# Kernel tuning notes

Hardware: AMD Instinct MI355X
Metric: run time of the kernel (lower is better)

Reference implementation:

```python
import jax, jax.numpy as jnp
import numpy as np

IN_DIM, HIDDEN, NCLASS = 128, 512, 10
BETA, THRESH = 0.9, 0.15


def setup_inputs() -> dict:
    key = jax.random.key(0)
    k_x, k_w1, k_w2 = jax.random.split(key, 3)
    B, T = 512, 512
    x = jax.random.uniform(k_x, (B, T, IN_DIM), dtype=jnp.float32)
    # kaiming_normal_(nonlinearity='linear'): std = 1/sqrt(fan_in); fc1 then scaled by 0.8
    W1 = jax.random.normal(k_w1, (HIDDEN, IN_DIM), dtype=jnp.float32) * (0.8 / np.sqrt(IN_DIM))
    b1 = jnp.zeros((HIDDEN,), dtype=jnp.float32)
    W2 = jax.random.normal(k_w2, (NCLASS, HIDDEN), dtype=jnp.float32) * (1.0 / np.sqrt(HIDDEN))
    b2 = jnp.zeros((NCLASS,), dtype=jnp.float32)
    return {"x": x, "W1": W1, "b1": b1, "W2": W2, "b2": b2}


def reference(x, W1, b1, W2, b2):
    B, T, D = x.shape
    xs = jnp.transpose(2.0 * x, (1, 0, 2))  # [T, B, D]

    def step(carry, xt):
        mem, acc = carry
        cur = xt @ W1.T + b1                      # [B, H]
        reset = (mem > THRESH).astype(cur.dtype)  # spike from previous mem (snntorch order)
        mem = BETA * mem + cur - reset * THRESH   # subtract reset
        spk = (mem > THRESH).astype(cur.dtype)
        acc = acc + spk @ W2.T + b2               # [B, C]
        return (mem, acc), None

    mem0 = jnp.zeros((B, HIDDEN), dtype=jnp.float32)
    acc0 = jnp.zeros((B, NCLASS), dtype=jnp.float32)
    (_, acc), _ = jax.lax.scan(step, (mem0, acc0), xs)
    return acc / T
```

## Files before the change

### kernel.cpp

```cpp
#include <hip/hip_runtime.h>

#define IN_DIM  128
#define HIDDEN  512
#define NCLASS  10
#define TSTEPS  512
#define BATCH   512
#define BETA    0.9f
#define THRESH  0.15f

typedef __attribute__((ext_vector_type(8))) short bf16x8;
typedef __attribute__((ext_vector_type(4))) float f32x4;

__device__ __forceinline__ unsigned short f2bf_rne(float f) {
    unsigned int u = __float_as_uint(f);
    u += 0x7FFFu + ((u >> 16) & 1u);
    return (unsigned short)(u >> 16);
}
__device__ __forceinline__ float bf2f(unsigned short h) {
    return __uint_as_float(((unsigned int)h) << 16);
}

__device__ __forceinline__ bf16x8 cvt8(const float4 a, const float4 b, float s) {
    float v[8] = {a.x * s, a.y * s, a.z * s, a.w * s,
                  b.x * s, b.y * s, b.z * s, b.w * s};
    bf16x8 o;
#pragma unroll
    for (int e = 0; e < 8; ++e) o[e] = (short)f2bf_rne(v[e]);
    return o;
}

__device__ __forceinline__ void cvt8s(const float4 a, const float4 b,
                                      bf16x8* hi, bf16x8* lo) {
    float v[8] = {a.x, a.y, a.z, a.w, b.x, b.y, b.z, b.w};
#pragma unroll
    for (int e = 0; e < 8; ++e) {
        unsigned short h = f2bf_rne(v[e]);
        (*hi)[e] = (short)h;
        (*lo)[e] = (short)f2bf_rne(v[e] - bf2f(h));
    }
}

__global__ __launch_bounds__(256, 4) void conv_x3(
    const float* __restrict__ x, unsigned short* __restrict__ xt)
{
    const int bid  = blockIdx.x;
    const int bblk = bid >> 9;
    const int t    = bid & 511;
    const int g    = threadIdx.x;
    const int kf   = g >> 6;
    const int i    = g & 63;
    const int l15  = i & 15;
    const int lg   = i >> 4;

    const float* src = x + ((size_t)(bblk * 16 + l15) * TSTEPS + t) * IN_DIM
                         + kf * 32 + lg * 8;
    const float4* p = reinterpret_cast<const float4*>(src);
    unsigned short* tile = xt + ((size_t)bblk * TSTEPS + t) * 2048;
    *(bf16x8*)(tile + g * 8) = cvt8(p[0], p[1], 2.0f);
}

__global__ __launch_bounds__(256, 1) void snn_mfma_a(
    const unsigned short* __restrict__ xt,
    const float* __restrict__ W1, const float* __restrict__ b1,
    float* __restrict__ cnt_ws)
{
    __shared__ char ring[8][4096];

    const int bid  = blockIdx.x;
    const int hblk = bid >> 5;
    const int bblk = bid & 31;
    const int b0   = bblk * 16;
    const int tid  = threadIdx.x;
    const int wave = tid >> 6;
    const int lane = tid & 63;
    const int l15  = lane & 15;
    const int lg   = lane >> 4;
    const int hbase = hblk * 64 + wave * 16;

    bf16x8 whi[4], wlo[4];
    {
        const float* wp = W1 + (size_t)(hbase + l15) * IN_DIM + lg * 8;
#pragma unroll
        for (int kf = 0; kf < 4; ++kf) {
            const float4* p = reinterpret_cast<const float4*>(wp + kf * 32);
            cvt8s(p[0], p[1], &whi[kf], &wlo[kf]);
        }
    }
    const float b1h = b1[hbase + l15];

    const char* gb = (const char*)xt + (size_t)bblk * TSTEPS * 4096;
    char* lsb = &ring[0][0];
    const int woff   = wave * 1024;
    const int lane16 = lane * 16;
    const unsigned lbase =
        (unsigned)(unsigned long long)(__attribute__((address_space(3))) char*)&ring[0][0]
        + (unsigned)lane16;

    f32x4 mem = {0.f, 0.f, 0.f, 0.f}, cnt = {0.f, 0.f, 0.f, 0.f};

#define STAGE(TT, SLOT)                                                        \
    {                                                                          \
        const char* g_ = gb + (size_t)(TT) * 4096 + woff + lane16;             \
        char* l_ = lsb + (SLOT) * 4096 + woff;                                 \
        __builtin_amdgcn_global_load_lds((const __attribute__((address_space(1))) void*)g_, (__attribute__((address_space(3))) void*)l_, 16, 0, 0); \
    }

#define RD1(OFF, DST)                                                          \
    asm volatile("ds_read_b128 %0, %1 offset:%c2"                              \
                 : "=&v"(DST) : "v"(lbase), "i"(OFF))

#define RD4A(S, F)                                                             \
    RD1((S) * 4096 + 0,    F[0]);                                              \
    RD1((S) * 4096 + 1024, F[1]);                                              \
    RD1((S) * 4096 + 2048, F[2]);                                              \
    RD1((S) * 4096 + 3072, F[3]);

#define MFMA_REC(F)                                                            \
    {                                                                          \
        f32x4 chh = {b1h, b1h, b1h, b1h};                                      \
        f32x4 chl = {0.f, 0.f, 0.f, 0.f};                                      \
        _Pragma("unroll")                                                      \
        for (int kf = 0; kf < 4; ++kf) {                                       \
            chh = __builtin_amdgcn_mfma_f32_16x16x32_bf16(F[kf], whi[kf], chh, 0, 0, 0); \
            chl = __builtin_amdgcn_mfma_f32_16x16x32_bf16(F[kf], wlo[kf], chl, 0, 0, 0); \
        }                                                                      \
        _Pragma("unroll")                                                      \
        for (int r = 0; r < 4; ++r) {                                          \
            float cur = chh[r] + chl[r];                                       \
            float dec = fmaf(BETA, mem[r], cur);                               \
            mem[r] = (mem[r] > THRESH) ? (dec - THRESH) : dec;                 \
            cnt[r] += (mem[r] > THRESH) ? 1.0f : 0.0f;                         \
        }                                                                      \
    }

#define ITER(J, CF, NF)                                                        \
    {                                                                          \
        asm volatile("s_waitcnt vmcnt(5)" ::: "memory");                       \
        __builtin_amdgcn_s_barrier();                                          \
        asm volatile("" ::: "memory");                                         \
        { int tt = tb + (J) + 7; if (tt > TSTEPS - 1) tt = TSTEPS - 1;         \
          STAGE(tt, ((J) + 7) & 7) }                                           \
        RD4A(((J) + 1) & 7, NF)                                                \
        asm volatile("s_waitcnt lgkmcnt(4)" ::: "memory");                     \
        __builtin_amdgcn_sched_barrier(0);                                     \
        MFMA_REC(CF)                                                           \
    }

    bf16x8 fA[4], fB[4];

    asm volatile("s_waitcnt vmcnt(0)" ::: "memory");
#pragma unroll
    for (int j = 0; j < 7; ++j)
        STAGE(j, j)
    asm volatile("s_waitcnt vmcnt(6)" ::: "memory");
    __builtin_amdgcn_s_barrier();
    asm volatile("" ::: "memory");
    RD4A(0, fA)

    for (int w = 0; w < TSTEPS / 8; ++w) {
        const int tb = w * 8;
        ITER(0, fA, fB)
        ITER(1, fB, fA)
        ITER(2, fA, fB)
        ITER(3, fB, fA)
        ITER(4, fA, fB)
        ITER(5, fB, fA)
        ITER(6, fA, fB)
        ITER(7, fB, fA)
    }
#undef ITER
#undef MFMA_REC
#undef RD4A
#undef RD1
#undef STAGE

    float* cp = cnt_ws + (size_t)b0 * HIDDEN + hbase + l15;
#pragma unroll
    for (int r = 0; r < 4; ++r)
        cp[(size_t)(lg * 4 + r) * HIDDEN] = cnt[r];
}

__global__ __launch_bounds__(256, 1) void snn_mfma_lds(
    const float* __restrict__ x, const float* __restrict__ W1,
    const float* __restrict__ b1, float* __restrict__ cnt_ws)
{
    __shared__ short ldsA[2][2][16 * IN_DIM];
    const int bid  = blockIdx.x;
    const int hblk = bid >> 5;
    const int bblk = bid & 31;
    const int b0   = bblk * 16;
    const int tid  = threadIdx.x;
    const int wave = tid >> 6;
    const int lane = tid & 63;
    const int l15  = lane & 15;
    const int lg   = lane >> 4;
    const int hbase = hblk * 64 + wave * 16;

    bf16x8 whi[4], wlo[4];
    {
        const float* wp = W1 + (size_t)(hbase + l15) * IN_DIM + lg * 8;
#pragma unroll
        for (int kf = 0; kf < 4; ++kf) {
            const float4* p = reinterpret_cast<const float4*>(wp + kf * 32);
            cvt8s(p[0], p[1], &whi[kf], &wlo[kf]);
        }
    }
    const float b1h = b1[hbase + l15];
    const int m_w  = wave * 4 + lg;
    const int widx = m_w * IN_DIM + ((l15 ^ (m_w & 7)) * 8);
    const float* xrow = x + ((size_t)(b0 + m_w) * TSTEPS) * IN_DIM + l15 * 8;
    int ridx[4];
#pragma unroll
    for (int kf = 0; kf < 4; ++kf)
        ridx[kf] = l15 * IN_DIM + (((lg + 4 * kf) ^ (l15 & 7)) * 8);

    f32x4 mem = {0.f, 0.f, 0.f, 0.f};
    f32x4 cnt = {0.f, 0.f, 0.f, 0.f};
    {
        const float4* p = reinterpret_cast<const float4*>(xrow);
        *(bf16x8*)&ldsA[0][0][widx] = cvt8(p[0], p[1], 2.0f);
    }
    float4 rA0, rA1, rB0, rB1;
    {
        const float4* p1 = reinterpret_cast<const float4*>(xrow + 1 * IN_DIM);
        rA0 = p1[0]; rA1 = p1[1];
        const float4* p2 = reinterpret_cast<const float4*>(xrow + 2 * IN_DIM);
        rB0 = p2[0]; rB1 = p2[1];
    }
    __syncthreads();

#define SNN_BODY(T_CUR, RC0, RC1)                                              \
    {                                                                          \
        const int buf = (T_CUR) & 1;                                           \
        if ((T_CUR) + 1 < TSTEPS) {                                            \
            *(bf16x8*)&ldsA[buf ^ 1][0][widx] = cvt8(RC0, RC1, 2.0f);          \
        }                                                                      \
        bf16x8 ahi[4];                                                         \
        _Pragma("unroll")                                                      \
        for (int kf = 0; kf < 4; ++kf)                                         \
            ahi[kf] = *(const bf16x8*)&ldsA[buf][0][ridx[kf]];                 \
        {                                                                      \
            int tld = (T_CUR) + 3;                                             \
            if (tld > TSTEPS - 1) tld = TSTEPS - 1;                            \
            const float4* p = reinterpret_cast<const float4*>(                 \
                xrow + (size_t)tld * IN_DIM);                                  \
            RC0 = p[0]; RC1 = p[1];                                            \
        }                                                                      \
        f32x4 chh = {b1h, b1h, b1h, b1h};                                      \
        f32x4 chl = {0.f, 0.f, 0.f, 0.f};                                      \
        _Pragma("unroll")                                                      \
        for (int kf = 0; kf < 4; ++kf) {                                       \
            chh = __builtin_amdgcn_mfma_f32_16x16x32_bf16(ahi[kf], whi[kf], chh, 0, 0, 0); \
            chl = __builtin_amdgcn_mfma_f32_16x16x32_bf16(ahi[kf], wlo[kf], chl, 0, 0, 0); \
        }                                                                      \
        _Pragma("unroll")                                                      \
        for (int r = 0; r < 4; ++r) {                                          \
            float cur = chh[r] + chl[r];                                       \
            float dec = fmaf(BETA, mem[r], cur);                               \
            mem[r] = (mem[r] > THRESH) ? (dec - THRESH) : dec;                 \
            cnt[r] += (mem[r] > THRESH) ? 1.0f : 0.0f;                         \
        }                                                                      \
        __syncthreads();                                                       \
    }

    for (int t = 0; t < TSTEPS; t += 2) {
        SNN_BODY(t,     rA0, rA1)
        SNN_BODY(t + 1, rB0, rB1)
    }
#undef SNN_BODY

    float* cp = cnt_ws + (size_t)b0 * HIDDEN + hbase + l15;
#pragma unroll
    for (int r = 0; r < 4; ++r)
        cp[(size_t)(lg * 4 + r) * HIDDEN] = cnt[r];
}

__global__ __launch_bounds__(64, 1) void snn_out(
    const float* __restrict__ cnt_ws, const float* __restrict__ W2,
    const float* __restrict__ b2, float* __restrict__ out)
{
    const int b = blockIdx.x;
    const int lane = threadIdx.x;
    float c8[8];
#pragma unroll
    for (int j = 0; j < 8; ++j)
        c8[j] = cnt_ws[(size_t)b * HIDDEN + lane + 64 * j];
#pragma unroll
    for (int c = 0; c < NCLASS; ++c) {
        float s = 0.f;
#pragma unroll
        for (int j = 0; j < 8; ++j)
            s = fmaf(c8[j], W2[c * HIDDEN + lane + 64 * j], s);
#pragma unroll
        for (int off = 32; off >= 1; off >>= 1)
            s += __shfl_xor(s, off, 64);
        if (lane == c)
            out[(size_t)b * NCLASS + c] = s * (1.0f / (float)TSTEPS) + b2[c];
    }
}

extern "C" void kernel_launch(void* const* d_in, const int* in_sizes, int n_in,
                              void* d_out, int out_size, void* d_ws, size_t ws_size,
                              hipStream_t stream) {
    const float* x  = (const float*)d_in[0];
    const float* W1 = (const float*)d_in[1];
    const float* b1 = (const float*)d_in[2];
    const float* W2 = (const float*)d_in[3];
    const float* b2 = (const float*)d_in[4];
    float* out = (float*)d_out;

    const size_t NX = (size_t)BATCH * TSTEPS * IN_DIM;
    float* cnt_ws = (float*)d_ws;
    unsigned short* xt = (unsigned short*)((char*)d_ws + (1u << 20));
    const size_t need = (1u << 20) + NX * sizeof(unsigned short);

    if (ws_size >= need) {
        conv_x3<<<dim3(32 * TSTEPS), dim3(256), 0, stream>>>(x, xt);
        snn_mfma_a<<<dim3(256), dim3(256), 0, stream>>>(xt, W1, b1, cnt_ws);
    } else {
        snn_mfma_lds<<<dim3(256), dim3(256), 0, stream>>>(x, W1, b1, cnt_ws);
    }
    snn_out<<<dim3(BATCH), dim3(64), 0, stream>>>(cnt_ws, W2, b2, out);
}
```

Measured before the change: 124.5 us.

## Enlarge LDS ring to 16 slots and barrier only every fourth timestep

```diff
diff --git a/kernel.cpp b/kernel.cpp
--- a/kernel.cpp
+++ b/kernel.cpp
@@ -64,7 +64,7 @@
     const float* __restrict__ W1, const float* __restrict__ b1,
     float* __restrict__ cnt_ws)
 {
-    __shared__ char ring[8][4096];
+    __shared__ char ring[16][4096];
 
     const int bid  = blockIdx.x;
     const int hblk = bid >> 5;
@@ -98,10 +98,10 @@
 
     f32x4 mem = {0.f, 0.f, 0.f, 0.f}, cnt = {0.f, 0.f, 0.f, 0.f};
 
-#define STAGE(TT, SLOT)                                                        \
+#define STAGE(TT)                                                              \
     {                                                                          \
         const char* g_ = gb + (size_t)(TT) * 4096 + woff + lane16;             \
-        char* l_ = lsb + (SLOT) * 4096 + woff;                                 \
+        char* l_ = lsb + ((TT) & 15) * 4096 + woff;                            \
         __builtin_amdgcn_global_load_lds((const __attribute__((address_space(1))) void*)g_, (__attribute__((address_space(3))) void*)l_, 16, 0, 0); \
     }
 
@@ -133,42 +133,47 @@
         }                                                                      \
     }
 
-#define ITER(J, CF, NF)                                                        \
-    {                                                                          \
-        asm volatile("s_waitcnt vmcnt(5)" ::: "memory");                       \
+#define ITER_B(J, CF, NF)                                                      \
+    {                                                                          \
+        asm volatile("s_waitcnt vmcnt(2)" ::: "memory");                       \
         __builtin_amdgcn_s_barrier();                                          \
         asm volatile("" ::: "memory");                                         \
-        { int tt = tb + (J) + 7; if (tt > TSTEPS - 1) tt = TSTEPS - 1;         \
-          STAGE(tt, ((J) + 7) & 7) }                                           \
-        RD4A(((J) + 1) & 7, NF)                                                \
+        STAGE(tb + (J) + 7)                                                    \
+        RD4A((tb + (J) + 1) & 15, NF)                                          \
         asm volatile("s_waitcnt lgkmcnt(4)" ::: "memory");                     \
         __builtin_amdgcn_sched_barrier(0);                                     \
         MFMA_REC(CF)                                                           \
     }
 
+#define ITER_N(J, CF, NF)                                                      \
+    {                                                                          \
+        STAGE(tb + (J) + 7)                                                    \
+        RD4A((tb + (J) + 1) & 15, NF)                                          \
+        asm volatile("s_waitcnt lgkmcnt(4)" ::: "memory");                     \
+        __builtin_amdgcn_sched_barrier(0);                                     \
+        MFMA_REC(CF)                                                           \
+    }
+
     bf16x8 fA[4], fB[4];
 
     asm volatile("s_waitcnt vmcnt(0)" ::: "memory");
 #pragma unroll
     for (int j = 0; j < 7; ++j)
-        STAGE(j, j)
+        STAGE(j)
     asm volatile("s_waitcnt vmcnt(6)" ::: "memory");
     __builtin_amdgcn_s_barrier();
     asm volatile("" ::: "memory");
     RD4A(0, fA)
 
-    for (int w = 0; w < TSTEPS / 8; ++w) {
-        const int tb = w * 8;
-        ITER(0, fA, fB)
-        ITER(1, fB, fA)
-        ITER(2, fA, fB)
-        ITER(3, fB, fA)
-        ITER(4, fA, fB)
-        ITER(5, fB, fA)
-        ITER(6, fA, fB)
-        ITER(7, fB, fA)
-    }
-#undef ITER
+    for (int w = 0; w < TSTEPS / 16; ++w) {
+        const int tb = w * 16;
+        ITER_B(0,  fA, fB)  ITER_N(1,  fB, fA)  ITER_N(2,  fA, fB)  ITER_N(3,  fB, fA)
+        ITER_B(4,  fA, fB)  ITER_N(5,  fB, fA)  ITER_N(6,  fA, fB)  ITER_N(7,  fB, fA)
+        ITER_B(8,  fA, fB)  ITER_N(9,  fB, fA)  ITER_N(10, fA, fB)  ITER_N(11, fB, fA)
+        ITER_B(12, fA, fB)  ITER_N(13, fB, fA)  ITER_N(14, fA, fB)  ITER_N(15, fB, fA)
+    }
+#undef ITER_B
+#undef ITER_N
 #undef MFMA_REC
 #undef RD4A
 #undef RD1
@@ -312,7 +317,7 @@
     const size_t NX = (size_t)BATCH * TSTEPS * IN_DIM;
     float* cnt_ws = (float*)d_ws;
     unsigned short* xt = (unsigned short*)((char*)d_ws + (1u << 20));
-    const size_t need = (1u << 20) + NX * sizeof(unsigned short);
+    const size_t need = (1u << 20) + (NX + 8 * 2048) * sizeof(unsigned short);
 
     if (ws_size >= need) {
         conv_x3<<<dim3(32 * TSTEPS), dim3(256), 0, stream>>>(x, xt);
```

Result: faster. 121.4 us (-2.5%).
